# Kernel tuning notes

Measured on AMD Instinct MI355X. Metric: run time of the kernel, lower is better.

Reference implementation:

```python
import jax, jax.numpy as jnp
import numpy as np

V, D, H, T, B = 32000, 256, 256, 128, 32
SOS = 126


def lstm_cell(x, h, c, Wih, Whh, bih, bhh):
    # torch LSTMCell gate order: i, f, g, o
    z = x @ Wih.T + bih + h @ Whh.T + bhh
    i, f, g, o = jnp.split(z, 4, axis=-1)
    c2 = jax.nn.sigmoid(f) * c + jax.nn.sigmoid(i) * jnp.tanh(g)
    h2 = jax.nn.sigmoid(o) * jnp.tanh(c2)
    return h2, c2


def setup_inputs() -> dict:
    key = jax.random.key(0)
    ks = jax.random.split(key, 22)
    s = 0.05
    rn = lambda k, shp: jax.random.normal(k, shp, jnp.float32) * s
    return {
        'x': jax.random.randint(ks[0], (B, T), 0, V),
        'emb_enc': rn(ks[1], (V, D)),
        'Wih_f': rn(ks[2], (4 * H, D)), 'Whh_f': rn(ks[3], (4 * H, H)),
        'bih_f': rn(ks[4], (4 * H,)), 'bhh_f': rn(ks[5], (4 * H,)),
        'Wih_b': rn(ks[6], (4 * H, D)), 'Whh_b': rn(ks[7], (4 * H, H)),
        'bih_b': rn(ks[8], (4 * H,)), 'bhh_b': rn(ks[9], (4 * H,)),
        'emb_dec': rn(ks[10], (V, D)),
        'Wa_h': rn(ks[11], (2 * H, 2 * H)), 'Wa_e': rn(ks[12], (2 * H, 2 * H)),
        'v_a': rn(ks[13], (2 * H,)), 'b_a': rn(ks[14], (2 * H,)),
        'Wih_d': rn(ks[15], (8 * H, D + 2 * H)), 'Whh_d': rn(ks[16], (8 * H, 2 * H)),
        'bih_d': rn(ks[17], (8 * H,)), 'bhh_d': rn(ks[18], (8 * H,)),
        'Wout': rn(ks[19], (V, 2 * H)), 'bout': rn(ks[20], (V,)),
    }


def reference(x, emb_enc, Wih_f, Whh_f, bih_f, bhh_f, Wih_b, Whh_b, bih_b, bhh_b,
              emb_dec, Wa_h, Wa_e, v_a, b_a, Wih_d, Whh_d, bih_d, bhh_d, Wout, bout):
    # ---- encoder: both directions stepped forward (module feeds one timestep at a time) ----
    h0 = jnp.zeros((B, H), jnp.float32)

    def enc_step(carry, tok):
        hf, cf, hb, cb = carry
        e = emb_enc[tok]                         # (B, D)
        hf, cf = lstm_cell(e, hf, cf, Wih_f, Whh_f, bih_f, bhh_f)
        hb, cb = lstm_cell(e, hb, cb, Wih_b, Whh_b, bih_b, bhh_b)
        return (hf, cf, hb, cb), jnp.concatenate([hf, hb], -1)

    (hf, cf, hb, cb), enc_out = jax.lax.scan(enc_step, (h0, h0, h0, h0), x.T)
    enc_out = enc_out.transpose(1, 0, 2)         # (B, T, 2H)
    proj_e = enc_out @ Wa_e.T                    # precompute attention key proj (B, T, 2H)

    # ---- decoder init: concat bidirectional final states ----
    h = jnp.concatenate([hf, hb], -1)            # (B, 2H)
    c = jnp.concatenate([cf, cb], -1)
    tok0 = jnp.full((B,), SOS, dtype=x.dtype)

    def dec_step(carry, _):
        h, c, tok = carry
        e = emb_dec[tok]                          # (B, D)
        q = h @ Wa_h.T                            # (B, 2H)
        energy = jnp.tanh(proj_e + q[:, None, :] + b_a) @ v_a   # (B, T)
        w = jax.nn.softmax(energy, axis=-1)
        ctx = jnp.einsum('bt,bth->bh', w, enc_out)
        h2, c2 = lstm_cell(jnp.concatenate([e, ctx], -1), h, c, Wih_d, Whh_d, bih_d, bhh_d)
        out = jax.nn.log_softmax(h2 @ Wout.T + bout, axis=-1)    # (B, V)
        nxt = jnp.argmax(out, axis=-1).astype(tok.dtype)
        return (h2, c2, nxt), out

    _, ys = jax.lax.scan(dec_step, (h, c, tok0), None, length=T)  # (T, B, V)
    return ys.transpose(1, 0, 2)                  # (B, T, V)
```

## Files before the change

kernel.cpp:

```cpp
#include <hip/hip_runtime.h>

#define V 32000
#define D 256
#define H 256
#define T 128
#define B 32
#define SOS 126
#define H2 512

__device__ __forceinline__ float sigf(float x) { return 1.f / (1.f + __expf(-x)); }
__device__ __forceinline__ float ftanh(float x) {
    x = fminf(15.f, fmaxf(-15.f, x));
    float e = __expf(2.f * x);
    return (e - 1.f) / (e + 1.f);
}

__global__ __launch_bounds__(256) void k_embed_t(const int* __restrict__ x,
                                                 const float* __restrict__ emb,
                                                 float* __restrict__ ET) {
    __shared__ float s[32][33];
    int t = blockIdx.x >> 3, kb = blockIdx.x & 7;
    int tid = threadIdx.x;
    int lk = tid & 31, lb = tid >> 5;
#pragma unroll
    for (int i = 0; i < 4; ++i) {
        int b = lb + i * 8;
        s[b][lk] = emb[x[b * T + t] * D + kb * 32 + lk];
    }
    __syncthreads();
    int lb2 = tid & 31, lk2 = tid >> 5;
#pragma unroll
    for (int i = 0; i < 4; ++i) {
        int k = lk2 + i * 8;
        ET[t * (D * B) + (kb * 32 + k) * B + lb2] = s[lb2][k];
    }
}

__global__ __launch_bounds__(256) void k_tr(const float* __restrict__ src,
                                            float* __restrict__ dst, int R, int C) {
    __shared__ float tle[32][33];
    int rb = blockIdx.x * 32, cb = blockIdx.y * 32;
    int lr = threadIdx.x & 31, lc = threadIdx.x >> 5;
#pragma unroll
    for (int i = 0; i < 32; i += 8) tle[lc + i][lr] = src[(size_t)(rb + lc + i) * C + cb + lr];
    __syncthreads();
#pragma unroll
    for (int i = 0; i < 32; i += 8) dst[(size_t)(cb + lc + i) * R + rb + lr] = tle[lr][lc + i];
}

__global__ __launch_bounds__(256) void k_prep_encw(
    const float* __restrict__ Wih_f, const float* __restrict__ Whh_f,
    const float* __restrict__ Wih_b, const float* __restrict__ Whh_b,
    float* __restrict__ WencT) {
    int idx = blockIdx.x * 256 + threadIdx.x;
    int k = idx >> 11, col = idx & 2047;
    int dir = col >> 10, cu = col & 1023;
    int u = cu >> 2, g = cu & 3;
    const float* Wih = dir ? Wih_b : Wih_f;
    const float* Whh = dir ? Whh_b : Whh_f;
    float v = (k < 256) ? Wih[(g * H + u) * D + k] : Whh[(g * H + u) * H + (k - 256)];
    WencT[idx] = v;
}

__global__ __launch_bounds__(256) void k_prep_decw(const float* __restrict__ Wih_d,
                                                   const float* __restrict__ Whh_d,
                                                   float* __restrict__ WdT) {
    int idx = blockIdx.x * 256 + threadIdx.x;
    int k = idx >> 11, col = idx & 2047;
    int u = col >> 2, g = col & 3;
    float v = (k < 768) ? Wih_d[(size_t)(g * H2 + u) * 768 + k]
                        : Whh_d[(size_t)(g * H2 + u) * H2 + (k - 768)];
    WdT[idx] = v;
}

__global__ __launch_bounds__(256) void k_enc_mm(
    const float* __restrict__ WencT, const float* __restrict__ ET,
    float* __restrict__ hencT, float* __restrict__ cencT, float* __restrict__ enc_out,
    const float* __restrict__ bih_f, const float* __restrict__ bhh_f,
    const float* __restrict__ bih_b, const float* __restrict__ bhh_b, int t) {
    __shared__ float zs[256 * 9];
    int tid = threadIdx.x;
    int rb = blockIdx.x & 7, bq = blockIdx.x >> 3;
    int pp = t & 1;
    int row = rb * 256 + tid;
    int dir = row >> 10, cu = row & 1023;
    int u = cu >> 2, g = cu & 3;
    int b0 = bq * 8;
    float bias = (dir ? bih_b : bih_f)[g * H + u] + (dir ? bhh_b : bhh_f)[g * H + u];

    float acc[8];
#pragma unroll
    for (int i = 0; i < 8; ++i) acc[i] = 0.f;
    const float* wp = WencT + row;
    const float* e0 = ET + t * (D * B) + b0;
    const float* h0p = hencT + pp * 16384 + dir * 8192 + b0;
#pragma unroll 4
    for (int k = 0; k < 256; ++k) {
        float w = wp[k * 2048];
#pragma unroll
        for (int i = 0; i < 8; ++i) acc[i] = fmaf(w, e0[k * 32 + i], acc[i]);
    }
#pragma unroll 4
    for (int k = 0; k < 256; ++k) {
        float w = wp[(256 + k) * 2048];
#pragma unroll
        for (int i = 0; i < 8; ++i) acc[i] = fmaf(w, h0p[k * 32 + i], acc[i]);
    }
#pragma unroll
    for (int i = 0; i < 8; ++i) zs[tid * 9 + i] = acc[i] + bias;
    __syncthreads();

#pragma unroll
    for (int j = 0; j < 2; ++j) {
        int item = tid + j * 256;
        int ul = item >> 3, bi = item & 7;
        float zi = zs[(ul * 4 + 0) * 9 + bi], zf = zs[(ul * 4 + 1) * 9 + bi];
        float zg = zs[(ul * 4 + 2) * 9 + bi], zo = zs[(ul * 4 + 3) * 9 + bi];
        int gu = (rb & 3) * 64 + ul;
        int b = b0 + bi;
        int ci = (dir * 256 + gu) * 32 + b;
        float c2 = sigf(zf) * cencT[ci] + sigf(zi) * ftanh(zg);
        cencT[ci] = c2;
        float h2 = sigf(zo) * ftanh(c2);
        hencT[(pp ^ 1) * 16384 + ci] = h2;
        enc_out[(b * T + t) * H2 + dir * H + gu] = h2;
    }
}

__global__ __launch_bounds__(256) void k_proj(const float* __restrict__ enc_out,
                                              const float* __restrict__ Wa_e,
                                              float* __restrict__ proj_e) {
    __shared__ float X[16][512];
    int tid = threadIdx.x;
    int r0 = blockIdx.x * 16;
    for (int i = tid; i < 16 * 512; i += 256) {
        int r = i >> 9, k = i & 511;
        X[r][k] = enc_out[(r0 + r) * H2 + k];
    }
    __syncthreads();
    int j0 = tid * 2;
    float acc0[16], acc1[16];
#pragma unroll
    for (int r = 0; r < 16; ++r) { acc0[r] = 0.f; acc1[r] = 0.f; }
    const float* w0 = Wa_e + j0 * H2;
    const float* w1 = Wa_e + (j0 + 1) * H2;
    for (int k = 0; k < H2; k += 4) {
        float4 wa = *(const float4*)(w0 + k);
        float4 wb = *(const float4*)(w1 + k);
#pragma unroll
        for (int r = 0; r < 16; ++r) {
            float4 xv = *(const float4*)(&X[r][k]);
            acc0[r] = fmaf(wa.x, xv.x, acc0[r]); acc0[r] = fmaf(wa.y, xv.y, acc0[r]);
            acc0[r] = fmaf(wa.z, xv.z, acc0[r]); acc0[r] = fmaf(wa.w, xv.w, acc0[r]);
            acc1[r] = fmaf(wb.x, xv.x, acc1[r]); acc1[r] = fmaf(wb.y, xv.y, acc1[r]);
            acc1[r] = fmaf(wb.z, xv.z, acc1[r]); acc1[r] = fmaf(wb.w, xv.w, acc1[r]);
        }
    }
#pragma unroll
    for (int r = 0; r < 16; ++r) {
        float2 st; st.x = acc0[r]; st.y = acc1[r];
        *(float2*)(proj_e + (r0 + r) * H2 + j0) = st;
    }
}

__global__ __launch_bounds__(256) void k_init_dec(const float* __restrict__ hencT,
                                                  const float* __restrict__ cencT,
                                                  float* __restrict__ hdecT,
                                                  float* __restrict__ cdecT) {
    int idx = blockIdx.x * 256 + threadIdx.x;
    hdecT[idx] = hencT[idx];
    cdecT[idx] = cencT[idx];
}

__global__ __launch_bounds__(256) void k_qinit(const float* __restrict__ hdecT,
                                               const float* __restrict__ WahT,
                                               float* __restrict__ q_buf) {
    int tid = threadIdx.x;
    int jb = blockIdx.x & 1, bh = blockIdx.x >> 1;
    int j = jb * 256 + tid, b0 = bh * 16;
    float acc[16];
#pragma unroll
    for (int i = 0; i < 16; ++i) acc[i] = 0.f;
    const float* wp = WahT + j;
    const float* xp = hdecT + b0;
#pragma unroll 4
    for (int k = 0; k < H2; ++k) {
        float w = wp[k * H2];
#pragma unroll
        for (int i = 0; i < 16; ++i) acc[i] = fmaf(w, xp[k * 32 + i], acc[i]);
    }
#pragma unroll
    for (int i = 0; i < 16; ++i) q_buf[(b0 + i) * H2 + j] = acc[i];
}

__global__ __launch_bounds__(512) void k_attn(
    const float* __restrict__ proj_e, const float* __restrict__ enc_out,
    const float* __restrict__ emb_dec, const float* __restrict__ q_buf,
    const float* __restrict__ b_a, const float* __restrict__ v_a,
    const float* __restrict__ Pm, const float* __restrict__ Ps, const int* __restrict__ Pi,
    float* __restrict__ lse, float* __restrict__ xcatT, int t, int finalize) {
    __shared__ float rm[512]; __shared__ float rs[512]; __shared__ int ri[512];
    __shared__ float es[128]; __shared__ float wsm[128]; __shared__ float sred[128];
    __shared__ int tok_sh;
    int tid = threadIdx.x;
    int b = blockIdx.x;
    int tokb = SOS;

    if (t > 0) {
        float m = -INFINITY, s = 0.f; int mi = 0x7fffffff;
        if (tid < 500) { m = Pm[tid * 32 + b]; s = Ps[tid * 32 + b]; mi = Pi[tid * 32 + b]; }
        rm[tid] = m; rs[tid] = s; ri[tid] = mi;
        __syncthreads();
        for (int off = 256; off >= 1; off >>= 1) {
            if (tid < off) {
                float m1 = rm[tid], m2 = rm[tid + off];
                float s1 = rs[tid], s2 = rs[tid + off];
                int i1 = ri[tid], i2 = ri[tid + off];
                float m_, s_; int i_;
                if (m2 > m1)      { m_ = m2; s_ = s2 + s1 * __expf(m1 - m2); i_ = i2; }
                else if (m1 > m2) { m_ = m1; s_ = s1 + s2 * __expf(m2 - m1); i_ = i1; }
                else              { m_ = m1; s_ = s1 + s2; i_ = (i1 < i2) ? i1 : i2; }
                rm[tid] = m_; rs[tid] = s_; ri[tid] = i_;
            }
            __syncthreads();
        }
        if (tid == 0) {
            lse[b * T + (t - 1)] = rm[0] + logf(rs[0]);
            tok_sh = ri[0];
        }
        __syncthreads();
        tokb = tok_sh;
    }
    if (finalize) return;

    if (tid < 256) xcatT[tid * 32 + b] = emb_dec[tokb * D + tid];

    int l = tid & 63, w = tid >> 6;
    float q8[8], va8[8];
    {
        const float* qp = q_buf + b * H2 + l * 8;
        const float* bp = b_a + l * 8;
        const float* vp = v_a + l * 8;
#pragma unroll
        for (int j = 0; j < 8; ++j) { q8[j] = qp[j] + bp[j]; va8[j] = vp[j]; }
    }
    for (int tt = w; tt < T; tt += 8) {
        const float* pp = proj_e + (b * T + tt) * H2 + l * 8;
        float s = 0.f;
#pragma unroll
        for (int j = 0; j < 8; ++j) s += ftanh(pp[j] + q8[j]) * va8[j];
#pragma unroll
        for (int off = 32; off >= 1; off >>= 1) s += __shfl_xor(s, off);
        if (l == 0) es[tt] = s;
    }
    __syncthreads();

    if (tid < 128) sred[tid] = es[tid];
    __syncthreads();
    for (int off = 64; off >= 1; off >>= 1) {
        if (tid < off) sred[tid] = fmaxf(sred[tid], sred[tid + off]);
        __syncthreads();
    }
    float M = sred[0];
    __syncthreads();
    float ev = 0.f;
    if (tid < 128) { ev = __expf(es[tid] - M); sred[tid] = ev; }
    __syncthreads();
    for (int off = 64; off >= 1; off >>= 1) {
        if (tid < off) sred[tid] += sred[tid + off];
        __syncthreads();
    }
    float S = sred[0];
    if (tid < 128) wsm[tid] = ev / S;
    __syncthreads();

    {
        int kk = tid;
        float acc = 0.f;
        const float* eo = enc_out + b * T * H2 + kk;
#pragma unroll 8
        for (int tt = 0; tt < T; ++tt) acc = fmaf(wsm[tt], eo[tt * H2], acc);
        xcatT[(256 + kk) * 32 + b] = acc;
    }
}

__global__ __launch_bounds__(256) void k_mm_dec(const float* __restrict__ WdT,
                                                const float* __restrict__ XdT,
                                                float* __restrict__ zp) {
    int tid = threadIdx.x;
    int bh = blockIdx.x & 1;
    int rb = (blockIdx.x >> 1) & 7;
    int ks = blockIdx.x >> 4;
    int row = rb * 256 + tid;
    int b0 = bh * 16;
    float acc[16];
#pragma unroll
    for (int i = 0; i < 16; ++i) acc[i] = 0.f;
    const float* wp = WdT + row;
    const float* xp = XdT + b0;
    int kbeg = ks * 160;
#pragma unroll 4
    for (int k = kbeg; k < kbeg + 160; ++k) {
        float w = wp[k * 2048];
#pragma unroll
        for (int i = 0; i < 16; ++i) acc[i] = fmaf(w, xp[k * 32 + i], acc[i]);
    }
    float* zo = zp + (size_t)(ks * 2048 + row) * 32 + b0;
#pragma unroll
    for (int i = 0; i < 16; i += 4) {
        float4 st; st.x = acc[i]; st.y = acc[i + 1]; st.z = acc[i + 2]; st.w = acc[i + 3];
        *(float4*)(zo + i) = st;
    }
}

__global__ __launch_bounds__(256) void k_cell_dec(const float* __restrict__ zp,
                                                  const float* __restrict__ bih_d,
                                                  const float* __restrict__ bhh_d,
                                                  float* __restrict__ cdecT,
                                                  float* __restrict__ hdecT) {
    int idx = blockIdx.x * 256 + threadIdx.x;
    int u = idx >> 5, b = idx & 31;
    float z[4];
#pragma unroll
    for (int g = 0; g < 4; ++g) {
        float s = 0.f;
#pragma unroll
        for (int ks = 0; ks < 8; ++ks) s += zp[(size_t)(ks * 2048 + u * 4 + g) * 32 + b];
        z[g] = s + bih_d[g * H2 + u] + bhh_d[g * H2 + u];
    }
    float cp = cdecT[u * 32 + b];
    float c2 = sigf(z[1]) * cp + sigf(z[0]) * ftanh(z[2]);
    cdecT[u * 32 + b] = c2;
    float h2 = sigf(z[3]) * ftanh(c2);
    hdecT[u * 32 + b] = h2;
}

__global__ __launch_bounds__(256) void k_logits(
    const float* __restrict__ WoutT, const float* __restrict__ WahT,
    const float* __restrict__ bout, const float* __restrict__ hdecT,
    float* __restrict__ out, float* __restrict__ q_buf,
    float* __restrict__ Pm, float* __restrict__ Ps, int* __restrict__ Pi, int t) {
    int tid = threadIdx.x;
    int bt = blockIdx.x & 1;
    int rblk = blockIdx.x >> 1;
    int row = rblk * 256 + tid;
    int b0 = bt * 16;
    const float* wp = (rblk < 125) ? (WoutT + row) : (WahT + (row - V));
    int wstride = (rblk < 125) ? V : H2;
    const float* xp = hdecT + b0;
    float acc[16];
#pragma unroll
    for (int i = 0; i < 16; ++i) acc[i] = 0.f;
#pragma unroll 4
    for (int k = 0; k < H2; ++k) {
        float w = wp[(size_t)k * wstride];
#pragma unroll
        for (int i = 0; i < 16; ++i) acc[i] = fmaf(w, xp[k * 32 + i], acc[i]);
    }
    if (rblk < 125) {
        float bo = bout[row];
        int l = tid & 63;
        int wt = rblk * 4 + (tid >> 6);
        float keep_m = 0.f, keep_s = 0.f; int keep_i = 0;
        for (int i = 0; i < 16; ++i) {
            float v = acc[i] + bo;
            out[((size_t)(b0 + i) * T + t) * V + row] = v;
            float m = v; int mi = row;
#pragma unroll
            for (int off = 1; off < 64; off <<= 1) {
                float om = __shfl_xor(m, off); int oi = __shfl_xor(mi, off);
                if (om > m || (om == m && oi < mi)) { m = om; mi = oi; }
            }
            float e = __expf(v - m);
#pragma unroll
            for (int off = 1; off < 64; off <<= 1) e += __shfl_xor(e, off);
            if (l == i) { keep_m = m; keep_i = mi; keep_s = e; }
        }
        if (l < 16) {
            Pm[wt * 32 + b0 + l] = keep_m;
            Ps[wt * 32 + b0 + l] = keep_s;
            Pi[wt * 32 + b0 + l] = keep_i;
        }
    } else {
        int jrow = row - V;
#pragma unroll
        for (int i = 0; i < 16; ++i) q_buf[(b0 + i) * H2 + jrow] = acc[i];
    }
}

__global__ __launch_bounds__(256) void k_norm(float* __restrict__ out,
                                              const float* __restrict__ lse) {
    const int total4 = B * T * V / 4;
    int stride = gridDim.x * 256;
    for (int i4 = blockIdx.x * 256 + threadIdx.x; i4 < total4; i4 += stride) {
        int rowv = i4 / (V / 4);
        float l = lse[rowv];
        float4* p = (float4*)out + i4;
        float4 v = *p;
        v.x -= l; v.y -= l; v.z -= l; v.w -= l;
        *p = v;
    }
}

extern "C" void kernel_launch(void* const* d_in, const int* in_sizes, int n_in,
                              void* d_out, int out_size, void* d_ws, size_t ws_size,
                              hipStream_t stream) {
    const int* x          = (const int*)d_in[0];
    const float* emb_enc  = (const float*)d_in[1];
    const float* Wih_f    = (const float*)d_in[2];
    const float* Whh_f    = (const float*)d_in[3];
    const float* bih_f    = (const float*)d_in[4];
    const float* bhh_f    = (const float*)d_in[5];
    const float* Wih_b    = (const float*)d_in[6];
    const float* Whh_b    = (const float*)d_in[7];
    const float* bih_b    = (const float*)d_in[8];
    const float* bhh_b    = (const float*)d_in[9];
    const float* emb_dec  = (const float*)d_in[10];
    const float* Wa_h     = (const float*)d_in[11];
    const float* Wa_e     = (const float*)d_in[12];
    const float* v_a      = (const float*)d_in[13];
    const float* b_a      = (const float*)d_in[14];
    const float* Wih_d    = (const float*)d_in[15];
    const float* Whh_d    = (const float*)d_in[16];
    const float* bih_d    = (const float*)d_in[17];
    const float* bhh_d    = (const float*)d_in[18];
    const float* Wout     = (const float*)d_in[19];
    const float* bout     = (const float*)d_in[20];
    float* out = (float*)d_out;

    float* ws = (float*)d_ws;
    size_t o = 0;
    float* ET      = ws + o; o += (size_t)T * D * B;
    float* enc_out = ws + o; o += (size_t)B * T * H2;
    float* proj_e  = ws + o; o += (size_t)B * T * H2;
    float* WoutT   = ws + o; o += (size_t)H2 * V;
    float* WdT     = ws + o; o += (size_t)1280 * 2048;
    float* WencT   = ws + o; o += (size_t)512 * 2048;
    float* WahT    = ws + o; o += (size_t)H2 * H2;
    float* hencT   = ws + o; o += 2 * 16384;
    float* cencT   = ws + o; o += 16384;
    float* xcatT   = ws + o; o += 1280 * 32;
    float* cdecT   = ws + o; o += 16384;
    float* q_buf   = ws + o; o += 16384;
    float* zp      = ws + o; o += (size_t)8 * 2048 * 32;
    float* Pm      = ws + o; o += 16000;
    float* Ps      = ws + o; o += 16000;
    float* lse     = ws + o; o += 4096;
    int*   Pi      = (int*)(ws + o); o += 16000;
    float* hdecT   = xcatT + 768 * 32;

    hipMemsetAsync(hencT, 0, (2 * 16384 + 16384) * sizeof(float), stream);
    k_embed_t<<<1024, 256, 0, stream>>>(x, emb_enc, ET);
    k_tr<<<dim3(1000, 16), 256, 0, stream>>>(Wout, WoutT, V, H2);
    k_tr<<<dim3(16, 16), 256, 0, stream>>>(Wa_h, WahT, H2, H2);
    k_prep_encw<<<4096, 256, 0, stream>>>(Wih_f, Whh_f, Wih_b, Whh_b, WencT);
    k_prep_decw<<<10240, 256, 0, stream>>>(Wih_d, Whh_d, WdT);

    for (int t = 0; t < T; ++t)
        k_enc_mm<<<32, 256, 0, stream>>>(WencT, ET, hencT, cencT, enc_out,
                                         bih_f, bhh_f, bih_b, bhh_b, t);
    k_proj<<<256, 256, 0, stream>>>(enc_out, Wa_e, proj_e);
    k_init_dec<<<64, 256, 0, stream>>>(hencT, cencT, hdecT, cdecT);
    k_qinit<<<4, 256, 0, stream>>>(hdecT, WahT, q_buf);

    for (int t = 0; t < T; ++t) {
        k_attn<<<32, 512, 0, stream>>>(proj_e, enc_out, emb_dec, q_buf, b_a, v_a,
                                       Pm, Ps, Pi, lse, xcatT, t, 0);
        k_mm_dec<<<128, 256, 0, stream>>>(WdT, xcatT, zp);
        k_cell_dec<<<64, 256, 0, stream>>>(zp, bih_d, bhh_d, cdecT, hdecT);
        k_logits<<<254, 256, 0, stream>>>(WoutT, WahT, bout, hdecT, out, q_buf,
                                          Pm, Ps, Pi, t);
    }
    k_attn<<<32, 512, 0, stream>>>(proj_e, enc_out, emb_dec, q_buf, b_a, v_a,
                                   Pm, Ps, Pi, lse, xcatT, T, 1);
    k_norm<<<4096, 256, 0, stream>>>(out, lse);
}
```

Baseline: 20.38 ms.

## Fuse encoder and decoder timestep loops into one persistent kernel with grid barriers

Replaces the hundreds of per-timestep kernel launches (encoder cell, attention, decoder matmul, cell, logits) with a single persistent 512-block kernel. Steps are separated by a hierarchical atomic grid barrier, and work is repartitioned across blocks using LDS-staged activations and split-K partial sums. It also fuses the embedding gather and the attention projection into the loop. The aim is to remove launch overhead and idle gaps between small dependent kernels. In exchange it needs all blocks co-resident for the spin barrier to make progress, and it carries a guard timeout that could silently break synchronization.

```diff
diff --git a/kernel.cpp b/kernel.cpp
--- a/kernel.cpp
+++ b/kernel.cpp
@@ -8,6 +8,12 @@
 #define SOS 126
 #define H2 512
 
+#define NBLK 512
+#define NTHR 256
+#define SCOPE __HIP_MEMORY_SCOPE_AGENT
+#define LDS_FLOATS 19456
+#define S0 18432
+
 __device__ __forceinline__ float sigf(float x) { return 1.f / (1.f + __expf(-x)); }
 __device__ __forceinline__ float ftanh(float x) {
     x = fminf(15.f, fmaxf(-15.f, x));
@@ -15,25 +21,29 @@
     return (e - 1.f) / (e + 1.f);
 }
 
-__global__ __launch_bounds__(256) void k_embed_t(const int* __restrict__ x,
-                                                 const float* __restrict__ emb,
-                                                 float* __restrict__ ET) {
-    __shared__ float s[32][33];
-    int t = blockIdx.x >> 3, kb = blockIdx.x & 7;
-    int tid = threadIdx.x;
-    int lk = tid & 31, lb = tid >> 5;
-#pragma unroll
-    for (int i = 0; i < 4; ++i) {
-        int b = lb + i * 8;
-        s[b][lk] = emb[x[b * T + t] * D + kb * 32 + lk];
+__device__ __forceinline__ void gbar(int* bar) {
+    __syncthreads();
+    if (threadIdx.x == 0) {
+        int g = __hip_atomic_load(bar + 17, __ATOMIC_RELAXED, SCOPE);
+        __threadfence();
+        int grp = (int)(blockIdx.x >> 5);
+        int a = __hip_atomic_fetch_add(bar + grp, 1, __ATOMIC_ACQ_REL, SCOPE);
+        if (a == 31) {
+            int r = __hip_atomic_fetch_add(bar + 16, 1, __ATOMIC_ACQ_REL, SCOPE);
+            if (r == 15) {
+                for (int i = 0; i < 17; ++i)
+                    __hip_atomic_store(bar + i, 0, __ATOMIC_RELAXED, SCOPE);
+                __hip_atomic_fetch_add(bar + 17, 1, __ATOMIC_RELEASE, SCOPE);
+            }
+        }
+        unsigned guard = 0;
+        while (__hip_atomic_load(bar + 17, __ATOMIC_RELAXED, SCOPE) == g) {
+            __builtin_amdgcn_s_sleep(2);
+            if (++guard > 800000000u) break;
+        }
+        (void)__hip_atomic_load(bar + 17, __ATOMIC_ACQUIRE, SCOPE);
     }
     __syncthreads();
-    int lb2 = tid & 31, lk2 = tid >> 5;
-#pragma unroll
-    for (int i = 0; i < 4; ++i) {
-        int k = lk2 + i * 8;
-        ET[t * (D * B) + (kb * 32 + k) * B + lb2] = s[lb2][k];
-    }
 }
 
 __global__ __launch_bounds__(256) void k_tr(const float* __restrict__ src,
@@ -73,321 +83,6 @@
     WdT[idx] = v;
 }
 
-__global__ __launch_bounds__(256) void k_enc_mm(
-    const float* __restrict__ WencT, const float* __restrict__ ET,
-    float* __restrict__ hencT, float* __restrict__ cencT, float* __restrict__ enc_out,
-    const float* __restrict__ bih_f, const float* __restrict__ bhh_f,
-    const float* __restrict__ bih_b, const float* __restrict__ bhh_b, int t) {
-    __shared__ float zs[256 * 9];
-    int tid = threadIdx.x;
-    int rb = blockIdx.x & 7, bq = blockIdx.x >> 3;
-    int pp = t & 1;
-    int row = rb * 256 + tid;
-    int dir = row >> 10, cu = row & 1023;
-    int u = cu >> 2, g = cu & 3;
-    int b0 = bq * 8;
-    float bias = (dir ? bih_b : bih_f)[g * H + u] + (dir ? bhh_b : bhh_f)[g * H + u];
-
-    float acc[8];
-#pragma unroll
-    for (int i = 0; i < 8; ++i) acc[i] = 0.f;
-    const float* wp = WencT + row;
-    const float* e0 = ET + t * (D * B) + b0;
-    const float* h0p = hencT + pp * 16384 + dir * 8192 + b0;
-#pragma unroll 4
-    for (int k = 0; k < 256; ++k) {
-        float w = wp[k * 2048];
-#pragma unroll
-        for (int i = 0; i < 8; ++i) acc[i] = fmaf(w, e0[k * 32 + i], acc[i]);
-    }
-#pragma unroll 4
-    for (int k = 0; k < 256; ++k) {
-        float w = wp[(256 + k) * 2048];
-#pragma unroll
-        for (int i = 0; i < 8; ++i) acc[i] = fmaf(w, h0p[k * 32 + i], acc[i]);
-    }
-#pragma unroll
-    for (int i = 0; i < 8; ++i) zs[tid * 9 + i] = acc[i] + bias;
-    __syncthreads();
-
-#pragma unroll
-    for (int j = 0; j < 2; ++j) {
-        int item = tid + j * 256;
-        int ul = item >> 3, bi = item & 7;
-        float zi = zs[(ul * 4 + 0) * 9 + bi], zf = zs[(ul * 4 + 1) * 9 + bi];
-        float zg = zs[(ul * 4 + 2) * 9 + bi], zo = zs[(ul * 4 + 3) * 9 + bi];
-        int gu = (rb & 3) * 64 + ul;
-        int b = b0 + bi;
-        int ci = (dir * 256 + gu) * 32 + b;
-        float c2 = sigf(zf) * cencT[ci] + sigf(zi) * ftanh(zg);
-        cencT[ci] = c2;
-        float h2 = sigf(zo) * ftanh(c2);
-        hencT[(pp ^ 1) * 16384 + ci] = h2;
-        enc_out[(b * T + t) * H2 + dir * H + gu] = h2;
-    }
-}
-
-__global__ __launch_bounds__(256) void k_proj(const float* __restrict__ enc_out,
-                                              const float* __restrict__ Wa_e,
-                                              float* __restrict__ proj_e) {
-    __shared__ float X[16][512];
-    int tid = threadIdx.x;
-    int r0 = blockIdx.x * 16;
-    for (int i = tid; i < 16 * 512; i += 256) {
-        int r = i >> 9, k = i & 511;
-        X[r][k] = enc_out[(r0 + r) * H2 + k];
-    }
-    __syncthreads();
-    int j0 = tid * 2;
-    float acc0[16], acc1[16];
-#pragma unroll
-    for (int r = 0; r < 16; ++r) { acc0[r] = 0.f; acc1[r] = 0.f; }
-    const float* w0 = Wa_e + j0 * H2;
-    const float* w1 = Wa_e + (j0 + 1) * H2;
-    for (int k = 0; k < H2; k += 4) {
-        float4 wa = *(const float4*)(w0 + k);
-        float4 wb = *(const float4*)(w1 + k);
-#pragma unroll
-        for (int r = 0; r < 16; ++r) {
-            float4 xv = *(const float4*)(&X[r][k]);
-            acc0[r] = fmaf(wa.x, xv.x, acc0[r]); acc0[r] = fmaf(wa.y, xv.y, acc0[r]);
-            acc0[r] = fmaf(wa.z, xv.z, acc0[r]); acc0[r] = fmaf(wa.w, xv.w, acc0[r]);
-            acc1[r] = fmaf(wb.x, xv.x, acc1[r]); acc1[r] = fmaf(wb.y, xv.y, acc1[r]);
-            acc1[r] = fmaf(wb.z, xv.z, acc1[r]); acc1[r] = fmaf(wb.w, xv.w, acc1[r]);
-        }
-    }
-#pragma unroll
-    for (int r = 0; r < 16; ++r) {
-        float2 st; st.x = acc0[r]; st.y = acc1[r];
-        *(float2*)(proj_e + (r0 + r) * H2 + j0) = st;
-    }
-}
-
-__global__ __launch_bounds__(256) void k_init_dec(const float* __restrict__ hencT,
-                                                  const float* __restrict__ cencT,
-                                                  float* __restrict__ hdecT,
-                                                  float* __restrict__ cdecT) {
-    int idx = blockIdx.x * 256 + threadIdx.x;
-    hdecT[idx] = hencT[idx];
-    cdecT[idx] = cencT[idx];
-}
-
-__global__ __launch_bounds__(256) void k_qinit(const float* __restrict__ hdecT,
-                                               const float* __restrict__ WahT,
-                                               float* __restrict__ q_buf) {
-    int tid = threadIdx.x;
-    int jb = blockIdx.x & 1, bh = blockIdx.x >> 1;
-    int j = jb * 256 + tid, b0 = bh * 16;
-    float acc[16];
-#pragma unroll
-    for (int i = 0; i < 16; ++i) acc[i] = 0.f;
-    const float* wp = WahT + j;
-    const float* xp = hdecT + b0;
-#pragma unroll 4
-    for (int k = 0; k < H2; ++k) {
-        float w = wp[k * H2];
-#pragma unroll
-        for (int i = 0; i < 16; ++i) acc[i] = fmaf(w, xp[k * 32 + i], acc[i]);
-    }
-#pragma unroll
-    for (int i = 0; i < 16; ++i) q_buf[(b0 + i) * H2 + j] = acc[i];
-}
-
-__global__ __launch_bounds__(512) void k_attn(
-    const float* __restrict__ proj_e, const float* __restrict__ enc_out,
-    const float* __restrict__ emb_dec, const float* __restrict__ q_buf,
-    const float* __restrict__ b_a, const float* __restrict__ v_a,
-    const float* __restrict__ Pm, const float* __restrict__ Ps, const int* __restrict__ Pi,
-    float* __restrict__ lse, float* __restrict__ xcatT, int t, int finalize) {
-    __shared__ float rm[512]; __shared__ float rs[512]; __shared__ int ri[512];
-    __shared__ float es[128]; __shared__ float wsm[128]; __shared__ float sred[128];
-    __shared__ int tok_sh;
-    int tid = threadIdx.x;
-    int b = blockIdx.x;
-    int tokb = SOS;
-
-    if (t > 0) {
-        float m = -INFINITY, s = 0.f; int mi = 0x7fffffff;
-        if (tid < 500) { m = Pm[tid * 32 + b]; s = Ps[tid * 32 + b]; mi = Pi[tid * 32 + b]; }
-        rm[tid] = m; rs[tid] = s; ri[tid] = mi;
-        __syncthreads();
-        for (int off = 256; off >= 1; off >>= 1) {
-            if (tid < off) {
-                float m1 = rm[tid], m2 = rm[tid + off];
-                float s1 = rs[tid], s2 = rs[tid + off];
-                int i1 = ri[tid], i2 = ri[tid + off];
-                float m_, s_; int i_;
-                if (m2 > m1)      { m_ = m2; s_ = s2 + s1 * __expf(m1 - m2); i_ = i2; }
-                else if (m1 > m2) { m_ = m1; s_ = s1 + s2 * __expf(m2 - m1); i_ = i1; }
-                else              { m_ = m1; s_ = s1 + s2; i_ = (i1 < i2) ? i1 : i2; }
-                rm[tid] = m_; rs[tid] = s_; ri[tid] = i_;
-            }
-            __syncthreads();
-        }
-        if (tid == 0) {
-            lse[b * T + (t - 1)] = rm[0] + logf(rs[0]);
-            tok_sh = ri[0];
-        }
-        __syncthreads();
-        tokb = tok_sh;
-    }
-    if (finalize) return;
-
-    if (tid < 256) xcatT[tid * 32 + b] = emb_dec[tokb * D + tid];
-
-    int l = tid & 63, w = tid >> 6;
-    float q8[8], va8[8];
-    {
-        const float* qp = q_buf + b * H2 + l * 8;
-        const float* bp = b_a + l * 8;
-        const float* vp = v_a + l * 8;
-#pragma unroll
-        for (int j = 0; j < 8; ++j) { q8[j] = qp[j] + bp[j]; va8[j] = vp[j]; }
-    }
-    for (int tt = w; tt < T; tt += 8) {
-        const float* pp = proj_e + (b * T + tt) * H2 + l * 8;
-        float s = 0.f;
-#pragma unroll
-        for (int j = 0; j < 8; ++j) s += ftanh(pp[j] + q8[j]) * va8[j];
-#pragma unroll
-        for (int off = 32; off >= 1; off >>= 1) s += __shfl_xor(s, off);
-        if (l == 0) es[tt] = s;
-    }
-    __syncthreads();
-
-    if (tid < 128) sred[tid] = es[tid];
-    __syncthreads();
-    for (int off = 64; off >= 1; off >>= 1) {
-        if (tid < off) sred[tid] = fmaxf(sred[tid], sred[tid + off]);
-        __syncthreads();
-    }
-    float M = sred[0];
-    __syncthreads();
-    float ev = 0.f;
-    if (tid < 128) { ev = __expf(es[tid] - M); sred[tid] = ev; }
-    __syncthreads();
-    for (int off = 64; off >= 1; off >>= 1) {
-        if (tid < off) sred[tid] += sred[tid + off];
-        __syncthreads();
-    }
-    float S = sred[0];
-    if (tid < 128) wsm[tid] = ev / S;
-    __syncthreads();
-
-    {
-        int kk = tid;
-        float acc = 0.f;
-        const float* eo = enc_out + b * T * H2 + kk;
-#pragma unroll 8
-        for (int tt = 0; tt < T; ++tt) acc = fmaf(wsm[tt], eo[tt * H2], acc);
-        xcatT[(256 + kk) * 32 + b] = acc;
-    }
-}
-
-__global__ __launch_bounds__(256) void k_mm_dec(const float* __restrict__ WdT,
-                                                const float* __restrict__ XdT,
-                                                float* __restrict__ zp) {
-    int tid = threadIdx.x;
-    int bh = blockIdx.x & 1;
-    int rb = (blockIdx.x >> 1) & 7;
-    int ks = blockIdx.x >> 4;
-    int row = rb * 256 + tid;
-    int b0 = bh * 16;
-    float acc[16];
-#pragma unroll
-    for (int i = 0; i < 16; ++i) acc[i] = 0.f;
-    const float* wp = WdT + row;
-    const float* xp = XdT + b0;
-    int kbeg = ks * 160;
-#pragma unroll 4
-    for (int k = kbeg; k < kbeg + 160; ++k) {
-        float w = wp[k * 2048];
-#pragma unroll
-        for (int i = 0; i < 16; ++i) acc[i] = fmaf(w, xp[k * 32 + i], acc[i]);
-    }
-    float* zo = zp + (size_t)(ks * 2048 + row) * 32 + b0;
-#pragma unroll
-    for (int i = 0; i < 16; i += 4) {
-        float4 st; st.x = acc[i]; st.y = acc[i + 1]; st.z = acc[i + 2]; st.w = acc[i + 3];
-        *(float4*)(zo + i) = st;
-    }
-}
-
-__global__ __launch_bounds__(256) void k_cell_dec(const float* __restrict__ zp,
-                                                  const float* __restrict__ bih_d,
-                                                  const float* __restrict__ bhh_d,
-                                                  float* __restrict__ cdecT,
-                                                  float* __restrict__ hdecT) {
-    int idx = blockIdx.x * 256 + threadIdx.x;
-    int u = idx >> 5, b = idx & 31;
-    float z[4];
-#pragma unroll
-    for (int g = 0; g < 4; ++g) {
-        float s = 0.f;
-#pragma unroll
-        for (int ks = 0; ks < 8; ++ks) s += zp[(size_t)(ks * 2048 + u * 4 + g) * 32 + b];
-        z[g] = s + bih_d[g * H2 + u] + bhh_d[g * H2 + u];
-    }
-    float cp = cdecT[u * 32 + b];
-    float c2 = sigf(z[1]) * cp + sigf(z[0]) * ftanh(z[2]);
-    cdecT[u * 32 + b] = c2;
-    float h2 = sigf(z[3]) * ftanh(c2);
-    hdecT[u * 32 + b] = h2;
-}
-
-__global__ __launch_bounds__(256) void k_logits(
-    const float* __restrict__ WoutT, const float* __restrict__ WahT,
-    const float* __restrict__ bout, const float* __restrict__ hdecT,
-    float* __restrict__ out, float* __restrict__ q_buf,
-    float* __restrict__ Pm, float* __restrict__ Ps, int* __restrict__ Pi, int t) {
-    int tid = threadIdx.x;
-    int bt = blockIdx.x & 1;
-    int rblk = blockIdx.x >> 1;
-    int row = rblk * 256 + tid;
-    int b0 = bt * 16;
-    const float* wp = (rblk < 125) ? (WoutT + row) : (WahT + (row - V));
-    int wstride = (rblk < 125) ? V : H2;
-    const float* xp = hdecT + b0;
-    float acc[16];
-#pragma unroll
-    for (int i = 0; i < 16; ++i) acc[i] = 0.f;
-#pragma unroll 4
-    for (int k = 0; k < H2; ++k) {
-        float w = wp[(size_t)k * wstride];
-#pragma unroll
-        for (int i = 0; i < 16; ++i) acc[i] = fmaf(w, xp[k * 32 + i], acc[i]);
-    }
-    if (rblk < 125) {
-        float bo = bout[row];
-        int l = tid & 63;
-        int wt = rblk * 4 + (tid >> 6);
-        float keep_m = 0.f, keep_s = 0.f; int keep_i = 0;
-        for (int i = 0; i < 16; ++i) {
-            float v = acc[i] + bo;
-            out[((size_t)(b0 + i) * T + t) * V + row] = v;
-            float m = v; int mi = row;
-#pragma unroll
-            for (int off = 1; off < 64; off <<= 1) {
-                float om = __shfl_xor(m, off); int oi = __shfl_xor(mi, off);
-                if (om > m || (om == m && oi < mi)) { m = om; mi = oi; }
-            }
-            float e = __expf(v - m);
-#pragma unroll
-            for (int off = 1; off < 64; off <<= 1) e += __shfl_xor(e, off);
-            if (l == i) { keep_m = m; keep_i = mi; keep_s = e; }
-        }
-        if (l < 16) {
-            Pm[wt * 32 + b0 + l] = keep_m;
-            Ps[wt * 32 + b0 + l] = keep_s;
-            Pi[wt * 32 + b0 + l] = keep_i;
-        }
-    } else {
-        int jrow = row - V;
-#pragma unroll
-        for (int i = 0; i < 16; ++i) q_buf[(b0 + i) * H2 + jrow] = acc[i];
-    }
-}
-
 __global__ __launch_bounds__(256) void k_norm(float* __restrict__ out,
                                               const float* __restrict__ lse) {
     const int total4 = B * T * V / 4;
@@ -399,6 +94,485 @@
         float4 v = *p;
         v.x -= l; v.y -= l; v.z -= l; v.w -= l;
         *p = v;
+    }
+}
+
+__global__ __launch_bounds__(256, 2) void k_seq(
+    const int* __restrict__ x, const float* __restrict__ emb_enc,
+    const float* __restrict__ emb_dec,
+    const float* __restrict__ bih_f, const float* __restrict__ bhh_f,
+    const float* __restrict__ bih_b, const float* __restrict__ bhh_b,
+    const float* __restrict__ bih_d, const float* __restrict__ bhh_d,
+    const float* __restrict__ Wa_e, const float* __restrict__ Wa_h,
+    const float* __restrict__ b_a, const float* __restrict__ v_a,
+    const float* __restrict__ bout,
+    const float* __restrict__ WencT, const float* __restrict__ WdT,
+    const float* __restrict__ WoutT, const float* __restrict__ WahT,
+    float* __restrict__ enc_out, float* __restrict__ proj_e,
+    float* __restrict__ cencT, float* __restrict__ zpenc,
+    float* __restrict__ hdecT, float* __restrict__ cdecT,
+    float* __restrict__ xcatT, float* __restrict__ q_buf, float* __restrict__ zp,
+    float* __restrict__ es_g, float* __restrict__ Pm, float* __restrict__ Ps,
+    int* __restrict__ Pi, float* __restrict__ lse, float* __restrict__ out,
+    int* bar) {
+    extern __shared__ float xs[];
+    const int blk = blockIdx.x, tid = threadIdx.x;
+    const int kc = (tid >> 3) & 7;
+    const int rp = (tid >> 6) * 8 + (tid & 7);
+
+    for (int t = 0; t <= T; ++t) {
+        if (blk < 128) {
+            int rowgrp = blk >> 2, c = (blk >> 1) & 1, bh = blk & 1;
+            int dir = rowgrp >> 4;
+            if (c == 0) {
+                if (t < T) {
+                    for (int i = tid; i < 4096; i += 256) {
+                        int bb = i >> 8, k = i & 255;
+                        int tok = x[(bh * 16 + bb) * T + t];
+                        xs[k * 20 + bb] = emb_enc[tok * 256 + k];
+                    }
+                }
+            } else {
+                if (t == 0) {
+                    for (int i = tid; i < 4096; i += 256) {
+                        int u = i >> 4, bb = i & 15;
+                        xs[u * 20 + bb] = 0.f;
+                    }
+                } else {
+                    bool writer = (rowgrp & 15) == 0;
+                    const float* zpp = zpenc + ((t - 1) & 1) * 131072;
+                    int pr = t & 1;
+                    for (int i = tid; i < 4096; i += 256) {
+                        int u = i >> 4, bb = i & 15, bG = bh * 16 + bb;
+                        int r = dir * 1024 + u * 4;
+                        float z[4];
+#pragma unroll
+                        for (int g = 0; g < 4; ++g) {
+                            float bias = (dir ? bih_b : bih_f)[g * 256 + u] +
+                                         (dir ? bhh_b : bhh_f)[g * 256 + u];
+                            z[g] = zpp[(size_t)(r + g) * 32 + bG] +
+                                   zpp[(size_t)(2048 + r + g) * 32 + bG] + bias;
+                        }
+                        int ci = ((pr * 2 + dir) * 256 + u) * 32 + bG;
+                        float cp = cencT[ci];
+                        float c2 = sigf(z[1]) * cp + sigf(z[0]) * ftanh(z[2]);
+                        float h2 = sigf(z[3]) * ftanh(c2);
+                        xs[u * 20 + bb] = h2;
+                        if (writer) {
+                            cencT[(((pr ^ 1) * 2 + dir) * 256 + u) * 32 + bG] = c2;
+                            enc_out[(size_t)(bG * T + (t - 1)) * H2 + dir * 256 + u] = h2;
+                            if (t == T) {
+                                hdecT[(dir * 256 + u) * 32 + bG] = h2;
+                                cdecT[(dir * 256 + u) * 32 + bG] = c2;
+                            }
+                        }
+                    }
+                }
+            }
+            __syncthreads();
+            if (t < T) {
+                int r0 = rowgrp * 64 + rp * 2;
+                float a0[16], a1[16];
+#pragma unroll
+                for (int j = 0; j < 16; ++j) { a0[j] = 0.f; a1[j] = 0.f; }
+#pragma unroll 4
+                for (int j = 0; j < 32; ++j) {
+                    int kl = kc + 8 * j;
+                    float2 w = *(const float2*)(WencT + (size_t)(c * 256 + kl) * 2048 + r0);
+                    const float* xp = xs + kl * 20;
+#pragma unroll
+                    for (int q = 0; q < 4; ++q) {
+                        float4 xv = *(const float4*)(xp + q * 4);
+                        a0[q*4+0] = fmaf(w.x, xv.x, a0[q*4+0]); a1[q*4+0] = fmaf(w.y, xv.x, a1[q*4+0]);
+                        a0[q*4+1] = fmaf(w.x, xv.y, a0[q*4+1]); a1[q*4+1] = fmaf(w.y, xv.y, a1[q*4+1]);
+                        a0[q*4+2] = fmaf(w.x, xv.z, a0[q*4+2]); a1[q*4+2] = fmaf(w.y, xv.z, a1[q*4+2]);
+                        a0[q*4+3] = fmaf(w.x, xv.w, a0[q*4+3]); a1[q*4+3] = fmaf(w.y, xv.w, a1[q*4+3]);
+                    }
+                }
+#pragma unroll
+                for (int j = 0; j < 16; ++j) {
+                    a0[j] += __shfl_xor(a0[j], 8); a0[j] += __shfl_xor(a0[j], 16); a0[j] += __shfl_xor(a0[j], 32);
+                    a1[j] += __shfl_xor(a1[j], 8); a1[j] += __shfl_xor(a1[j], 16); a1[j] += __shfl_xor(a1[j], 32);
+                }
+                if (((tid >> 3) & 7) == 0) {
+                    float* zb = zpenc + (t & 1) * 131072 + (size_t)(c * 2048 + r0) * 32 + bh * 16;
+#pragma unroll
+                    for (int q = 0; q < 4; ++q) {
+                        *(float4*)(zb + q * 4)      = make_float4(a0[q*4], a0[q*4+1], a0[q*4+2], a0[q*4+3]);
+                        *(float4*)(zb + 32 + q * 4) = make_float4(a1[q*4], a1[q*4+1], a1[q*4+2], a1[q*4+3]);
+                    }
+                }
+            }
+        }
+        gbar(bar);
+    }
+
+    {
+        if (blk < 256) {
+            int r0 = blk * 16;
+            for (int i = tid; i < 16 * 512; i += 256) {
+                int r = i >> 9, k = i & 511;
+                xs[r * 512 + k] = enc_out[(size_t)(r0 + r) * H2 + k];
+            }
+            __syncthreads();
+            int j0 = tid * 2;
+            float acc0[16], acc1[16];
+#pragma unroll
+            for (int r = 0; r < 16; ++r) { acc0[r] = 0.f; acc1[r] = 0.f; }
+            const float* w0 = Wa_e + j0 * H2;
+            const float* w1 = Wa_e + (j0 + 1) * H2;
+            for (int k = 0; k < H2; k += 4) {
+                float4 wa = *(const float4*)(w0 + k);
+                float4 wb = *(const float4*)(w1 + k);
+#pragma unroll
+                for (int r = 0; r < 16; ++r) {
+                    float4 xv = *(const float4*)(&xs[r * 512 + k]);
+                    acc0[r] = fmaf(wa.x, xv.x, acc0[r]); acc0[r] = fmaf(wa.y, xv.y, acc0[r]);
+                    acc0[r] = fmaf(wa.z, xv.z, acc0[r]); acc0[r] = fmaf(wa.w, xv.w, acc0[r]);
+                    acc1[r] = fmaf(wb.x, xv.x, acc1[r]); acc1[r] = fmaf(wb.y, xv.y, acc1[r]);
+                    acc1[r] = fmaf(wb.z, xv.z, acc1[r]); acc1[r] = fmaf(wb.w, xv.w, acc1[r]);
+                }
+            }
+#pragma unroll
+            for (int r = 0; r < 16; ++r) {
+                float2 st; st.x = acc0[r]; st.y = acc1[r];
+                *(float2*)(proj_e + (size_t)(r0 + r) * H2 + j0) = st;
+            }
+        } else if (blk < 320) {
+            int gi = (blk - 256) * 256 + tid;
+            int j = gi >> 5, b = gi & 31;
+            float a0 = 0, a1 = 0, a2 = 0, a3 = 0;
+            const float* wr = Wa_h + (size_t)j * H2;
+            for (int k = 0; k < H2; k += 4) {
+                float4 w = *(const float4*)(wr + k);
+                a0 = fmaf(w.x, hdecT[(k    ) * 32 + b], a0);
+                a1 = fmaf(w.y, hdecT[(k + 1) * 32 + b], a1);
+                a2 = fmaf(w.z, hdecT[(k + 2) * 32 + b], a2);
+                a3 = fmaf(w.w, hdecT[(k + 3) * 32 + b], a3);
+            }
+            q_buf[b * H2 + j] = (a0 + a1) + (a2 + a3);
+        }
+    }
+    gbar(bar);
+
+    for (int t = 0; t < T; ++t) {
+        if (blk < 32) {
+            int b = blk;
+            float* rm = xs + S0; float* rs = rm + 256; int* ri = (int*)(rs + 256);
+            int tok = SOS;
+            if (t > 0) {
+                float m = -INFINITY, s = 0.f; int mi = 0x7fffffff;
+                for (int i = tid; i < 512; i += 256) {
+                    if (i < 500) {
+                        float m2 = Pm[b * 512 + i], s2 = Ps[b * 512 + i];
+                        int i2 = Pi[b * 512 + i];
+                        if (m2 > m)      { s = s2 + s * __expf(m - m2); m = m2; mi = i2; }
+                        else if (m > m2) { s = s + s2 * __expf(m2 - m); }
+                        else             { s = s + s2; mi = (mi < i2) ? mi : i2; }
+                    }
+                }
+                rm[tid] = m; rs[tid] = s; ri[tid] = mi;
+                __syncthreads();
+                for (int off = 128; off >= 1; off >>= 1) {
+                    if (tid < off) {
+                        float m1 = rm[tid], m2 = rm[tid + off];
+                        float s1 = rs[tid], s2 = rs[tid + off];
+                        int i1 = ri[tid], i2 = ri[tid + off];
+                        float m_, s_; int i_;
+                        if (m2 > m1)      { m_ = m2; s_ = s2 + s1 * __expf(m1 - m2); i_ = i2; }
+                        else if (m1 > m2) { m_ = m1; s_ = s1 + s2 * __expf(m2 - m1); i_ = i1; }
+                        else              { m_ = m1; s_ = s1 + s2; i_ = (i1 < i2) ? i1 : i2; }
+                        rm[tid] = m_; rs[tid] = s_; ri[tid] = i_;
+                    }
+                    __syncthreads();
+                }
+                if (tid == 0) lse[b * T + (t - 1)] = rm[0] + logf(rs[0]);
+                __syncthreads();
+                tok = ri[0];
+            }
+            xcatT[tid * 32 + b] = emb_dec[tok * 256 + tid];
+        } else {
+            int w = (blk - 32) * 4 + (tid >> 6);
+            int l = tid & 63;
+            float4 ba0 = *(const float4*)(b_a + l * 8);
+            float4 ba1 = *(const float4*)(b_a + l * 8 + 4);
+            float4 va0 = *(const float4*)(v_a + l * 8);
+            float4 va1 = *(const float4*)(v_a + l * 8 + 4);
+            for (int task = w; task < 4096; task += 1920) {
+                int b = task >> 7, tt = task & 127;
+                float4 q0 = *(const float4*)(q_buf + b * H2 + l * 8);
+                float4 q1 = *(const float4*)(q_buf + b * H2 + l * 8 + 4);
+                const float* pp = proj_e + (size_t)(b * T + tt) * H2 + l * 8;
+                float4 p0 = *(const float4*)(pp);
+                float4 p1 = *(const float4*)(pp + 4);
+                float s = ftanh(p0.x + q0.x + ba0.x) * va0.x + ftanh(p0.y + q0.y + ba0.y) * va0.y
+                        + ftanh(p0.z + q0.z + ba0.z) * va0.z + ftanh(p0.w + q0.w + ba0.w) * va0.w
+                        + ftanh(p1.x + q1.x + ba1.x) * va1.x + ftanh(p1.y + q1.y + ba1.y) * va1.y
+                        + ftanh(p1.z + q1.z + ba1.z) * va1.z + ftanh(p1.w + q1.w + ba1.w) * va1.w;
+#pragma unroll
+                for (int off = 32; off >= 1; off >>= 1) s += __shfl_xor(s, off);
+                if (l == 0) es_g[b * 128 + tt] = s;
+            }
+        }
+        gbar(bar);
+
+        if (blk < 32) {
+            int b = blk;
+            float* es = xs + S0; float* red = es + 128; float* wsm = red + 128;
+            if (tid < 128) { es[tid] = es_g[b * 128 + tid]; red[tid] = es[tid]; }
+            __syncthreads();
+            for (int off = 64; off >= 1; off >>= 1) {
+                if (tid < off) red[tid] = fmaxf(red[tid], red[tid + off]);
+                __syncthreads();
+            }
+            float M = red[0];
+            __syncthreads();
+            float ev = 0.f;
+            if (tid < 128) { ev = __expf(es[tid] - M); red[tid] = ev; }
+            __syncthreads();
+            for (int off = 64; off >= 1; off >>= 1) {
+                if (tid < off) red[tid] += red[tid + off];
+                __syncthreads();
+            }
+            float S = red[0];
+            __syncthreads();
+            if (tid < 128) wsm[tid] = ev / S;
+            __syncthreads();
+            float acc0 = 0.f, acc1 = 0.f;
+            const float* eo = enc_out + (size_t)b * T * H2;
+#pragma unroll 8
+            for (int t2 = 0; t2 < T; ++t2) {
+                float wv = wsm[t2];
+                acc0 = fmaf(wv, eo[t2 * H2 + tid], acc0);
+                acc1 = fmaf(wv, eo[t2 * H2 + tid + 256], acc1);
+            }
+            xcatT[(256 + tid) * 32 + b] = acc0;
+            xcatT[(512 + tid) * 32 + b] = acc1;
+        } else if (blk >= 64 && blk < 192) {
+            int idx = blk - 64;
+            int rowgrp = idx >> 2, ch = (idx >> 1) & 1, bh = idx & 1;
+            const float* src = hdecT + (size_t)ch * 256 * 32;
+            for (int i4 = tid; i4 < 1024; i4 += 256) {
+                int k = i4 >> 2, b4 = (i4 & 3) * 4;
+                *(float4*)(xs + k * 20 + b4) = *(const float4*)(src + k * 32 + bh * 16 + b4);
+            }
+            __syncthreads();
+            int r0 = rowgrp * 64 + rp * 2;
+            int kOFF = 768 + ch * 256;
+            float a0[16], a1[16];
+#pragma unroll
+            for (int j = 0; j < 16; ++j) { a0[j] = 0.f; a1[j] = 0.f; }
+#pragma unroll 4
+            for (int j = 0; j < 32; ++j) {
+                int kl = kc + 8 * j;
+                float2 w = *(const float2*)(WdT + (size_t)(kOFF + kl) * 2048 + r0);
+                const float* xp = xs + kl * 20;
+#pragma unroll
+                for (int q = 0; q < 4; ++q) {
+                    float4 xv = *(const float4*)(xp + q * 4);
+                    a0[q*4+0] = fmaf(w.x, xv.x, a0[q*4+0]); a1[q*4+0] = fmaf(w.y, xv.x, a1[q*4+0]);
+                    a0[q*4+1] = fmaf(w.x, xv.y, a0[q*4+1]); a1[q*4+1] = fmaf(w.y, xv.y, a1[q*4+1]);
+                    a0[q*4+2] = fmaf(w.x, xv.z, a0[q*4+2]); a1[q*4+2] = fmaf(w.y, xv.z, a1[q*4+2]);
+                    a0[q*4+3] = fmaf(w.x, xv.w, a0[q*4+3]); a1[q*4+3] = fmaf(w.y, xv.w, a1[q*4+3]);
+                }
+            }
+#pragma unroll
+            for (int j = 0; j < 16; ++j) {
+                a0[j] += __shfl_xor(a0[j], 8); a0[j] += __shfl_xor(a0[j], 16); a0[j] += __shfl_xor(a0[j], 32);
+                a1[j] += __shfl_xor(a1[j], 8); a1[j] += __shfl_xor(a1[j], 16); a1[j] += __shfl_xor(a1[j], 32);
+            }
+            if (((tid >> 3) & 7) == 0) {
+                float* zb = zp + (size_t)((3 + ch) * 2048 + r0) * 32 + bh * 16;
+#pragma unroll
+                for (int q = 0; q < 4; ++q) {
+                    *(float4*)(zb + q * 4)      = make_float4(a0[q*4], a0[q*4+1], a0[q*4+2], a0[q*4+3]);
+                    *(float4*)(zb + 32 + q * 4) = make_float4(a1[q*4], a1[q*4+1], a1[q*4+2], a1[q*4+3]);
+                }
+            }
+        }
+        gbar(bar);
+
+        if (blk < 192) {
+            int rowgrp = blk / 6, rem = blk % 6;
+            int ch = rem >> 1, bh = rem & 1;
+            const float* src = xcatT + (size_t)ch * 256 * 32;
+            for (int i4 = tid; i4 < 1024; i4 += 256) {
+                int k = i4 >> 2, b4 = (i4 & 3) * 4;
+                *(float4*)(xs + k * 20 + b4) = *(const float4*)(src + k * 32 + bh * 16 + b4);
+            }
+            __syncthreads();
+            int r0 = rowgrp * 64 + rp * 2;
+            int kOFF = ch * 256;
+            float a0[16], a1[16];
+#pragma unroll
+            for (int j = 0; j < 16; ++j) { a0[j] = 0.f; a1[j] = 0.f; }
+#pragma unroll 4
+            for (int j = 0; j < 32; ++j) {
+                int kl = kc + 8 * j;
+                float2 w = *(const float2*)(WdT + (size_t)(kOFF + kl) * 2048 + r0);
+                const float* xp = xs + kl * 20;
+#pragma unroll
+                for (int q = 0; q < 4; ++q) {
+                    float4 xv = *(const float4*)(xp + q * 4);
+                    a0[q*4+0] = fmaf(w.x, xv.x, a0[q*4+0]); a1[q*4+0] = fmaf(w.y, xv.x, a1[q*4+0]);
+                    a0[q*4+1] = fmaf(w.x, xv.y, a0[q*4+1]); a1[q*4+1] = fmaf(w.y, xv.y, a1[q*4+1]);
+                    a0[q*4+2] = fmaf(w.x, xv.z, a0[q*4+2]); a1[q*4+2] = fmaf(w.y, xv.z, a1[q*4+2]);
+                    a0[q*4+3] = fmaf(w.x, xv.w, a0[q*4+3]); a1[q*4+3] = fmaf(w.y, xv.w, a1[q*4+3]);
+                }
+            }
+#pragma unroll
+            for (int j = 0; j < 16; ++j) {
+                a0[j] += __shfl_xor(a0[j], 8); a0[j] += __shfl_xor(a0[j], 16); a0[j] += __shfl_xor(a0[j], 32);
+                a1[j] += __shfl_xor(a1[j], 8); a1[j] += __shfl_xor(a1[j], 16); a1[j] += __shfl_xor(a1[j], 32);
+            }
+            if (((tid >> 3) & 7) == 0) {
+                float* zb = zp + (size_t)(ch * 2048 + r0) * 32 + bh * 16;
+#pragma unroll
+                for (int q = 0; q < 4; ++q) {
+                    *(float4*)(zb + q * 4)      = make_float4(a0[q*4], a0[q*4+1], a0[q*4+2], a0[q*4+3]);
+                    *(float4*)(zb + 32 + q * 4) = make_float4(a1[q*4], a1[q*4+1], a1[q*4+2], a1[q*4+3]);
+                }
+            }
+        }
+        gbar(bar);
+
+        if (blk < 64) {
+            int i = blk * 256 + tid;
+            int u = i >> 5, b = i & 31;
+            float z[4];
+#pragma unroll
+            for (int g = 0; g < 4; ++g) {
+                float s = bih_d[g * H2 + u] + bhh_d[g * H2 + u];
+#pragma unroll
+                for (int c = 0; c < 5; ++c) s += zp[(size_t)(c * 2048 + u * 4 + g) * 32 + b];
+                z[g] = s;
+            }
+            float cp = cdecT[u * 32 + b];
+            float c2 = sigf(z[1]) * cp + sigf(z[0]) * ftanh(z[2]);
+            cdecT[u * 32 + b] = c2;
+            hdecT[u * 32 + b] = sigf(z[3]) * ftanh(c2);
+        }
+        gbar(bar);
+
+        if (blk < 508) {
+            for (int i4 = tid; i4 < 4096; i4 += 256) {
+                int k = i4 >> 3, b4 = (i4 & 7) * 4;
+                *(float4*)(xs + k * 36 + b4) = *(const float4*)(hdecT + k * 32 + b4);
+            }
+            __syncthreads();
+            bool isQ = (blk >= 500);
+            const float* wb = isQ ? (WahT + (blk - 500) * 64) : (WoutT + blk * 64);
+            const int wst = isQ ? H2 : V;
+            int rp2 = rp * 2;
+            float a0[32], a1[32];
+#pragma unroll
+            for (int j = 0; j < 32; ++j) { a0[j] = 0.f; a1[j] = 0.f; }
+#pragma unroll 4
+            for (int kk = 0; kk < 64; ++kk) {
+                int k = kc + 8 * kk;
+                float2 w = *(const float2*)(wb + (size_t)k * wst + rp2);
+                const float* xp = xs + k * 36;
+#pragma unroll
+                for (int q = 0; q < 8; ++q) {
+                    float4 xv = *(const float4*)(xp + q * 4);
+                    a0[q*4+0] = fmaf(w.x, xv.x, a0[q*4+0]); a1[q*4+0] = fmaf(w.y, xv.x, a1[q*4+0]);
+                    a0[q*4+1] = fmaf(w.x, xv.y, a0[q*4+1]); a1[q*4+1] = fmaf(w.y, xv.y, a1[q*4+1]);
+                    a0[q*4+2] = fmaf(w.x, xv.z, a0[q*4+2]); a1[q*4+2] = fmaf(w.y, xv.z, a1[q*4+2]);
+                    a0[q*4+3] = fmaf(w.x, xv.w, a0[q*4+3]); a1[q*4+3] = fmaf(w.y, xv.w, a1[q*4+3]);
+                }
+            }
+#pragma unroll
+            for (int j = 0; j < 32; ++j) {
+                a0[j] += __shfl_xor(a0[j], 8); a0[j] += __shfl_xor(a0[j], 16); a0[j] += __shfl_xor(a0[j], 32);
+                a1[j] += __shfl_xor(a1[j], 8); a1[j] += __shfl_xor(a1[j], 16); a1[j] += __shfl_xor(a1[j], 32);
+            }
+            __syncthreads();
+            if (!isQ) {
+                if (((tid >> 3) & 7) == 0) {
+#pragma unroll
+                    for (int j = 0; j < 32; ++j) {
+                        xs[(rp2    ) * 37 + j] = a0[j];
+                        xs[(rp2 + 1) * 37 + j] = a1[j];
+                    }
+                }
+                __syncthreads();
+                int row0 = blk * 64;
+                {
+                    int r = tid & 63, bo = tid >> 6;
+                    float bv = bout[row0 + r];
+#pragma unroll
+                    for (int e = 0; e < 8; ++e) {
+                        int b = bo * 8 + e;
+                        out[((size_t)(b * T) + t) * V + row0 + r] = xs[r * 37 + b] + bv;
+                    }
+                }
+                float* pm8 = xs + S0; float* ps8 = pm8 + 256; int* pi8 = (int*)(ps8 + 256);
+                {
+                    int g = tid >> 5, b = tid & 31;
+                    float m = -INFINITY, s = 0.f; int mi = 0;
+#pragma unroll
+                    for (int i = 0; i < 8; ++i) {
+                        int rr = g * 8 + i;
+                        float v = xs[rr * 37 + b] + bout[row0 + rr];
+                        if (v > m) { s *= __expf(m - v); m = v; mi = row0 + rr; }
+                        s += __expf(v - m);
+                    }
+                    pm8[g * 32 + b] = m; ps8[g * 32 + b] = s; pi8[g * 32 + b] = mi;
+                }
+                __syncthreads();
+                if (tid < 32) {
+                    int b = tid;
+                    float m = pm8[b], s = ps8[b]; int mi = pi8[b];
+#pragma unroll
+                    for (int g = 1; g < 8; ++g) {
+                        float m2 = pm8[g * 32 + b], s2 = ps8[g * 32 + b]; int i2 = pi8[g * 32 + b];
+                        if (m2 > m)      { s = s2 + s * __expf(m - m2); m = m2; mi = i2; }
+                        else if (m > m2) { s = s + s2 * __expf(m2 - m); }
+                        else             { s = s + s2; mi = (mi < i2) ? mi : i2; }
+                    }
+                    Pm[b * 512 + blk] = m; Ps[b * 512 + blk] = s; Pi[b * 512 + blk] = mi;
+                }
+            } else {
+                if (((tid >> 3) & 7) == 0) {
+                    int j0 = (blk - 500) * 64 + rp2;
+#pragma unroll
+                    for (int b = 0; b < 32; ++b) {
+                        q_buf[b * H2 + j0]     = a0[b];
+                        q_buf[b * H2 + j0 + 1] = a1[b];
+                    }
+                }
+            }
+        }
+        gbar(bar);
+    }
+
+    if (blk < 32) {
+        int b = blk;
+        float* rm = xs + S0; float* rs = rm + 256; int* ri = (int*)(rs + 256);
+        float m = -INFINITY, s = 0.f; int mi = 0x7fffffff;
+        for (int i = tid; i < 512; i += 256) {
+            if (i < 500) {
+                float m2 = Pm[b * 512 + i], s2 = Ps[b * 512 + i]; int i2 = Pi[b * 512 + i];
+                if (m2 > m)      { s = s2 + s * __expf(m - m2); m = m2; mi = i2; }
+                else if (m > m2) { s = s + s2 * __expf(m2 - m); }
+                else             { s = s + s2; mi = (mi < i2) ? mi : i2; }
+            }
+        }
+        rm[tid] = m; rs[tid] = s; ri[tid] = mi;
+        __syncthreads();
+        for (int off = 128; off >= 1; off >>= 1) {
+            if (tid < off) {
+                float m1 = rm[tid], m2 = rm[tid + off];
+                float s1 = rs[tid], s2 = rs[tid + off];
+                float m_, s_;
+                if (m2 > m1)      { m_ = m2; s_ = s2 + s1 * __expf(m1 - m2); }
+                else if (m1 > m2) { m_ = m1; s_ = s1 + s2 * __expf(m2 - m1); }
+                else              { m_ = m1; s_ = s1 + s2; }
+                rm[tid] = m_; rs[tid] = s_;
+            }
+            __syncthreads();
+        }
+        if (tid == 0) lse[b * T + (T - 1)] = rm[0] + logf(rs[0]);
     }
 }
 
@@ -430,48 +604,42 @@
 
     float* ws = (float*)d_ws;
     size_t o = 0;
-    float* ET      = ws + o; o += (size_t)T * D * B;
     float* enc_out = ws + o; o += (size_t)B * T * H2;
     float* proj_e  = ws + o; o += (size_t)B * T * H2;
     float* WoutT   = ws + o; o += (size_t)H2 * V;
     float* WdT     = ws + o; o += (size_t)1280 * 2048;
     float* WencT   = ws + o; o += (size_t)512 * 2048;
     float* WahT    = ws + o; o += (size_t)H2 * H2;
-    float* hencT   = ws + o; o += 2 * 16384;
-    float* cencT   = ws + o; o += 16384;
-    float* xcatT   = ws + o; o += 1280 * 32;
+    float* cencT   = ws + o; o += 2 * 2 * 256 * 32;
+    float* zpenc   = ws + o; o += 2 * 2 * 2048 * 32;
+    float* hdecT   = ws + o; o += 16384;
     float* cdecT   = ws + o; o += 16384;
+    float* xcatT   = ws + o; o += 768 * 32;
     float* q_buf   = ws + o; o += 16384;
-    float* zp      = ws + o; o += (size_t)8 * 2048 * 32;
-    float* Pm      = ws + o; o += 16000;
-    float* Ps      = ws + o; o += 16000;
-    float* lse     = ws + o; o += 4096;
-    int*   Pi      = (int*)(ws + o); o += 16000;
-    float* hdecT   = xcatT + 768 * 32;
-
-    hipMemsetAsync(hencT, 0, (2 * 16384 + 16384) * sizeof(float), stream);
-    k_embed_t<<<1024, 256, 0, stream>>>(x, emb_enc, ET);
+    float* zp      = ws + o; o += (size_t)5 * 2048 * 32;
+    float* es_g    = ws + o; o += 32 * 128;
+    float* Pm      = ws + o; o += 32 * 512;
+    float* Ps      = ws + o; o += 32 * 512;
+    float* lse     = ws + o; o += 32 * 128;
+    int*   Pi      = (int*)(ws + o); o += 32 * 512;
+    int*   bar     = (int*)(ws + o); o += 256;
+
+    hipMemsetAsync(cencT, 0, 2 * 2 * 256 * 32 * sizeof(float), stream);
+    hipMemsetAsync(bar, 0, 256 * sizeof(int), stream);
+
     k_tr<<<dim3(1000, 16), 256, 0, stream>>>(Wout, WoutT, V, H2);
     k_tr<<<dim3(16, 16), 256, 0, stream>>>(Wa_h, WahT, H2, H2);
     k_prep_encw<<<4096, 256, 0, stream>>>(Wih_f, Whh_f, Wih_b, Whh_b, WencT);
     k_prep_decw<<<10240, 256, 0, stream>>>(Wih_d, Whh_d, WdT);
 
-    for (int t = 0; t < T; ++t)
-        k_enc_mm<<<32, 256, 0, stream>>>(WencT, ET, hencT, cencT, enc_out,
-                                         bih_f, bhh_f, bih_b, bhh_b, t);
-    k_proj<<<256, 256, 0, stream>>>(enc_out, Wa_e, proj_e);
-    k_init_dec<<<64, 256, 0, stream>>>(hencT, cencT, hdecT, cdecT);
-    k_qinit<<<4, 256, 0, stream>>>(hdecT, WahT, q_buf);
-
-    for (int t = 0; t < T; ++t) {
-        k_attn<<<32, 512, 0, stream>>>(proj_e, enc_out, emb_dec, q_buf, b_a, v_a,
-                                       Pm, Ps, Pi, lse, xcatT, t, 0);
-        k_mm_dec<<<128, 256, 0, stream>>>(WdT, xcatT, zp);
-        k_cell_dec<<<64, 256, 0, stream>>>(zp, bih_d, bhh_d, cdecT, hdecT);
-        k_logits<<<254, 256, 0, stream>>>(WoutT, WahT, bout, hdecT, out, q_buf,
-                                          Pm, Ps, Pi, t);
-    }
-    k_attn<<<32, 512, 0, stream>>>(proj_e, enc_out, emb_dec, q_buf, b_a, v_a,
-                                   Pm, Ps, Pi, lse, xcatT, T, 1);
+    k_seq<<<NBLK, NTHR, LDS_FLOATS * sizeof(float), stream>>>(
+        x, emb_enc, emb_dec,
+        bih_f, bhh_f, bih_b, bhh_b, bih_d, bhh_d,
+        Wa_e, Wa_h, b_a, v_a, bout,
+        WencT, WdT, WoutT, WahT,
+        enc_out, proj_e, cencT, zpenc,
+        hdecT, cdecT, xcatT, q_buf, zp,
+        es_g, Pm, Ps, Pi, lse, out, bar);
+
     k_norm<<<4096, 256, 0, stream>>>(out, lse);
 }
```

After: 57.58 ms. 183% more time.
